# Kernel optimization log

Measured on AMD Instinct MI355X. Metric: run time of the kernel, lower is better.

The kernel has to match this reference:

```python
import jax, jax.numpy as jnp
import numpy as np

LEAK = 0.1   # LeakyReLU negative slope used by Conv2dBatchLeaky
EPS = 1e-5   # BatchNorm eps (torch default)


def conv_bn_leaky(x, w, gamma, beta, mean, var, stride, pad):
    # Conv2d(bias=False) -> BatchNorm (inference) -> LeakyReLU(0.1)
    y = jax.lax.conv_general_dilated(
        x, w, (stride, stride), [(pad, pad), (pad, pad)],
        dimension_numbers=("NCHW", "OIHW", "NCHW"))
    scale = gamma / jnp.sqrt(var + EPS)
    shift = beta - mean * scale
    y = y * scale[None, :, None, None] + shift[None, :, None, None]
    return jnp.where(y > 0, y, LEAK * y)


def reorg(x, s):
    # lightnet Reorg: exact permutation of the darknet reorg layer
    B, C, H, W = x.shape
    x = x.reshape(B, C, H // s, s, W // s, s)
    x = x.transpose(0, 3, 5, 1, 2, 4)           # (B, s, s, C, H/s, W/s)
    return x.reshape(B, s * s * C, H // s, W // s)


def setup_inputs() -> dict:
    key = jax.random.key(0)
    ks = jax.random.split(key, 13)
    B = 64
    inp = {
        "feat0": jax.random.normal(ks[0], (B, 1024, 19, 19), jnp.float32),
        "feat1": jax.random.normal(ks[1], (B, 512, 38, 38), jnp.float32),
        "w1": jax.random.normal(ks[2], (64, 512, 1, 1), jnp.float32) * 0.05,
        "g1": jax.random.uniform(ks[3], (64,), jnp.float32, 0.5, 1.5),
        "b1": jax.random.normal(ks[4], (64,), jnp.float32) * 0.1,
        "m1": jax.random.normal(ks[5], (64,), jnp.float32) * 0.1,
        "v1": jax.random.uniform(ks[6], (64,), jnp.float32, 0.5, 1.5),
        "w2": jax.random.normal(ks[7], (1024, 1280, 3, 3), jnp.float32) * 0.02,
        "g2": jax.random.uniform(ks[8], (1024,), jnp.float32, 0.5, 1.5),
        "b2": jax.random.normal(ks[9], (1024,), jnp.float32) * 0.1,
        "m2": jax.random.normal(ks[10], (1024,), jnp.float32) * 0.1,
        "v2": jax.random.uniform(ks[11], (1024,), jnp.float32, 0.5, 1.5),
        # meta_state: (num_classes=20, num_anchors*6=30, 1024+1)
        "reweight": jax.random.normal(ks[12], (20, 30, 1025), jnp.float32) * 0.05,
    }
    return inp


def reference(feat0, feat1, w1, g1, b1, m1, v1, w2, g2, b2, m2, v2, reweight):
    # layers[0]: 1x1 ConvBatchLeaky(512->64) + Reorg(2)
    x = conv_bn_leaky(feat1, w1, g1, b1, m1, v1, stride=1, pad=0)
    x = reorg(x, 2)                                  # (B, 256, 19, 19)
    # layers[1]: 3x3 ConvBatchLeaky(1280->1024), pad=1
    cat = jnp.concatenate([x, feat0], axis=1)        # (B, 1280, 19, 19)
    pre = conv_bn_leaky(cat, w2, g2, b2, m2, v2, stride=1, pad=1)  # (B,1024,19,19)
    # get_reweighted_output: per-class dynamic 1x1 conv, batched as one einsum
    cw = reweight[:, :, :-1]                         # (K=20, O=30, 1024)
    cb = reweight[:, :, -1]                          # (K, O)
    det = jnp.einsum("bchw,koc->bkohw", pre, cw) + cb[None, :, :, None, None]
    B, _, _, H, W = det.shape
    return det.reshape(B * 20, 30, H, W)
```

## Files before the change

kernel.cpp:

```cpp
#include <hip/hip_runtime.h>

typedef unsigned short u16;
typedef __attribute__((ext_vector_type(8))) __bf16 bf16x8;
typedef __attribute__((ext_vector_type(4))) float f32x4;

__device__ __forceinline__ u16 f2bf(float f) {
  union { float f; unsigned u; } v; v.f = f;
  unsigned r = v.u + 0x7fffu + ((v.u >> 16) & 1u);
  return (u16)(r >> 16);
}

__device__ __forceinline__ void gld16(const void* g, const void* l) {
  __builtin_amdgcn_global_load_lds((const __attribute__((address_space(1))) void*)g,
                                   (__attribute__((address_space(3))) void*)l, 16, 0, 0);
}

#define BARX() do { asm volatile("" ::: "memory"); __builtin_amdgcn_s_barrier(); \
                    asm volatile("" ::: "memory"); } while (0)
#define LGKM0() do { asm volatile("s_waitcnt lgkmcnt(0)" ::: "memory"); \
                     __builtin_amdgcn_sched_barrier(0); } while (0)

__global__ __launch_bounds__(256) void k_prep_small(
    const float* w1, const float* rw,
    const float* g1, const float* b1, const float* m1, const float* v1,
    const float* g2, const float* b2, const float* m2, const float* v2,
    u16* w1b, u16* cwt,
    float* scale1, float* shift1, float* scale2, float* shift2, float* cbf)
{
  int i = blockIdx.x * 256 + threadIdx.x;
  if (i < 32768) { w1b[i] = f2bf(w1[i]); return; }
  i -= 32768;
  if (i < 655360) {
    int n = i >> 10, c = i & 1023;
    cwt[i] = (n < 600) ? f2bf(rw[n * 1025 + c]) : (u16)0;
    return;
  }
  i -= 655360;
  if (i < 64) {
    float s = g1[i] * rsqrtf(v1[i] + 1e-5f);
    scale1[i] = s; shift1[i] = b1[i] - m1[i] * s;
  } else if (i < 1088) {
    int c = i - 64;
    float s = g2[c] * rsqrtf(v2[c] + 1e-5f);
    scale2[c] = s; shift2[c] = b2[c] - m2[c] * s;
  } else if (i < 1728) {
    int n = i - 1088;
    cbf[n] = (n < 600) ? rw[n * 1025 + 1024] : 0.f;
  }
}

__global__ __launch_bounds__(256) void k_prep_w2(const float* w2, u16* w2t) {
  __shared__ float buf[11520];
  int o = blockIdx.x;
  const float* src = w2 + (size_t)o * 11520;
  for (int i = threadIdx.x; i < 11520; i += 256) buf[i] = src[i];
  __syncthreads();
  for (int t = 0; t < 9; ++t) {
    int dy = t / 3, dx = t - dy * 3;
    u16* dst = w2t + ((size_t)dy * 1024 + o) * 3840 + dx * 1280;
    for (int ci = threadIdx.x; ci < 1280; ci += 256) dst[ci] = f2bf(buf[ci * 9 + t]);
  }
}

__global__ __launch_bounds__(256) void k_feat0(const float* feat0, u16* cat) {
  __shared__ float tile[32][33];
  int b = blockIdx.z, c0 = blockIdx.y * 32, p0 = blockIdx.x * 32;
  int tid = threadIdx.x;
  int lo = tid & 31, hi = tid >> 5;
#pragma unroll
  for (int pass = 0; pass < 4; ++pass) {
    int cl = pass * 8 + hi;
    int p = p0 + lo;
    tile[cl][lo] = (p < 361) ? feat0[((size_t)(b * 1024 + c0 + cl)) * 361 + p] : 0.f;
  }
  __syncthreads();
#pragma unroll
  for (int pass = 0; pass < 4; ++pass) {
    int pl = pass * 8 + hi;
    int p = p0 + pl;
    if (p < 361) {
      int h = p / 19, w = p - h * 19;
      cat[(((size_t)b * 21 + 1 + h) * 21 + 1 + w) * 1280 + 256 + c0 + lo] = f2bf(tile[lo][pl]);
    }
  }
}

__global__ __launch_bounds__(256) void k_conv1(const float* feat1, const u16* w1b,
    const float* scale1, const float* shift1, u16* cat)
{
  __shared__ u16 As[128 * 40];
  __shared__ u16 Bs[64 * 32];
  int tid = threadIdx.x;
  int wave = tid >> 6, lane = tid & 63;
  int wr = wave >> 1, wc = wave & 1;
  int lm = lane & 15, lq = lane >> 4;
  int m0 = blockIdx.x * 128;

  int mLoc = tid & 127, cHalf = tid >> 7;
  int mA = m0 + mLoc;
  int bA = mA / 1444, qA = mA - bA * 1444;
  const float* aG = feat1 + ((size_t)bA * 512) * 1444 + qA;

  const u16* bG = w1b + (tid >> 2) * 512 + (tid & 3) * 8;
  char* BsW = (char*)Bs + wave * 1024;

  f32x4 acc[4][2];
#pragma unroll
  for (int i = 0; i < 4; ++i)
#pragma unroll
    for (int j = 0; j < 2; ++j)
#pragma unroll
      for (int r = 0; r < 4; ++r) acc[i][j][r] = 0.f;

  for (int k0 = 0; k0 < 512; k0 += 32) {
    gld16(bG + k0, BsW);
#pragma unroll
    for (int pass = 0; pass < 16; ++pass) {
      int c = pass * 2 + cHalf;
      As[mLoc * 40 + c] = f2bf(aG[(size_t)(k0 + c) * 1444]);
    }
    __syncthreads();
    bf16x8 aF[4], bF[2];
#pragma unroll
    for (int i = 0; i < 4; ++i)
      aF[i] = *(const bf16x8*)(As + (wr * 64 + i * 16 + lm) * 40 + lq * 8);
#pragma unroll
    for (int j = 0; j < 2; ++j)
      bF[j] = *(const bf16x8*)(Bs + (wc * 32 + j * 16 + lm) * 32 + lq * 8);
#pragma unroll
    for (int i = 0; i < 4; ++i)
#pragma unroll
      for (int j = 0; j < 2; ++j)
        acc[i][j] = __builtin_amdgcn_mfma_f32_16x16x32_bf16(aF[i], bF[j], acc[i][j], 0, 0, 0);
    __syncthreads();
  }

  int o0 = wc * 32;
  float sc[2], sh[2];
#pragma unroll
  for (int j = 0; j < 2; ++j) {
    int o = o0 + j * 16 + lm;
    sc[j] = scale1[o]; sh[j] = shift1[o];
  }
#pragma unroll
  for (int i = 0; i < 4; ++i) {
#pragma unroll
    for (int r = 0; r < 4; ++r) {
      int m = m0 + wr * 64 + i * 16 + lq * 4 + r;
      int b = m / 1444, q = m - b * 1444;
      int yy = q / 38, xx = q - yy * 38;
      size_t base = (((size_t)b * 21 + 1 + (yy >> 1)) * 21 + 1 + (xx >> 1)) * 1280
                  + ((yy & 1) * 2 + (xx & 1)) * 64;
#pragma unroll
      for (int j = 0; j < 2; ++j) {
        float v = acc[i][j][r] * sc[j] + sh[j];
        v = v > 0.f ? v : 0.1f * v;
        cat[base + o0 + j * 16 + lm] = f2bf(v);
      }
    }
  }
}

__global__ __launch_bounds__(512) void k_conv2(const u16* cat, const u16* w2t,
    const float* scale2, const float* shift2, u16* pre)
{
  __shared__ __align__(16) u16 As[2][16384];
  __shared__ __align__(16) u16 Bs[2][8192];

  int tid = threadIdx.x;
  int wave = tid >> 6, lane = tid & 63;
  int wr = wave >> 1, wc = wave & 1;
  int lm = lane & 15, lq = lane >> 4;
  int n0 = (blockIdx.x & 7) * 128;
  int m0 = (blockIdx.x >> 3) * 256;

  int rsub = tid >> 3;
  int cOff = ((tid & 7) ^ (rsub & 7)) * 8;

  const u16* aBase[4];
#pragma unroll
  for (int r = 0; r < 4; ++r) {
    int m = m0 + r * 64 + rsub; if (m > 23103) m = 23103;
    int b = m / 361, pq = m - b * 361, y = pq / 19, x = pq - y * 19;
    aBase[r] = cat + ((size_t)(b * 21 + y) * 21 + x) * 1280 + cOff;
  }
  const u16* bBase[2];
#pragma unroll
  for (int r = 0; r < 2; ++r)
    bBase[r] = w2t + (size_t)(n0 + r * 64 + rsub) * 3840 + cOff;

  int c0 = ((0 + lq) ^ (lm & 7)) * 8;
  int c1 = ((4 + lq) ^ (lm & 7)) * 8;
  const u16* aRd = &As[0][(wr * 64 + lm) * 64];
  const u16* bRd = &Bs[0][(wc * 64 + lm) * 64];

  f32x4 acc[4][4];
#pragma unroll
  for (int i = 0; i < 4; ++i)
#pragma unroll
    for (int j = 0; j < 4; ++j)
#pragma unroll
      for (int r = 0; r < 4; ++r) acc[i][j][r] = 0.f;

  auto stageA = [&](int p, int aOff) {
#pragma unroll
    for (int r = 0; r < 4; ++r)
      gld16(aBase[r] + aOff, &As[p][r * 4096 + wave * 512]);
  };
  auto stageB = [&](int p, size_t bOff) {
#pragma unroll
    for (int r = 0; r < 2; ++r)
      gld16(bBase[r] + bOff, &Bs[p][r * 4096 + wave * 512]);
  };

  stageA(0, 0);        stageB(0, 0);
  stageA(1, 64);       stageB(1, 64);
  asm volatile("s_waitcnt vmcnt(6)" ::: "memory");
  __builtin_amdgcn_sched_barrier(0);
  BARX();

  int dyS = 0, koS = 128;

  for (int kt = 0; kt < 180; ++kt) {
    int p = kt & 1;
    const u16* A = aRd + p * 16384;
    const u16* B = bRd + p * 8192;
    bool pf = (kt + 2 < 180);
    int aOff = dyS * 26880 + koS;
    size_t bOff = (size_t)dyS * 3932160 + koS;

    bf16x8 aF[4][2], bF[4][2];

#pragma unroll
    for (int i = 0; i < 2; ++i) {
      aF[i][0] = *(const bf16x8*)(A + i * 1024 + c0);
      aF[i][1] = *(const bf16x8*)(A + i * 1024 + c1);
    }
#pragma unroll
    for (int j = 0; j < 2; ++j) {
      bF[j][0] = *(const bf16x8*)(B + j * 1024 + c0);
      bF[j][1] = *(const bf16x8*)(B + j * 1024 + c1);
    }
    BARX();
    LGKM0();
    __builtin_amdgcn_s_setprio(1);
#pragma unroll
    for (int i = 0; i < 2; ++i)
#pragma unroll
      for (int j = 0; j < 2; ++j) {
        acc[i][j] = __builtin_amdgcn_mfma_f32_16x16x32_bf16(aF[i][0], bF[j][0], acc[i][j], 0, 0, 0);
        acc[i][j] = __builtin_amdgcn_mfma_f32_16x16x32_bf16(aF[i][1], bF[j][1], acc[i][j], 0, 0, 0);
      }
    __builtin_amdgcn_s_setprio(0);
    BARX();

#pragma unroll
    for (int i = 2; i < 4; ++i) {
      aF[i][0] = *(const bf16x8*)(A + i * 1024 + c0);
      aF[i][1] = *(const bf16x8*)(A + i * 1024 + c1);
    }
    BARX();
    LGKM0();
    __builtin_amdgcn_s_setprio(1);
#pragma unroll
    for (int i = 2; i < 4; ++i)
#pragma unroll
      for (int j = 0; j < 2; ++j) {
        acc[i][j] = __builtin_amdgcn_mfma_f32_16x16x32_bf16(aF[i][0], bF[j][0], acc[i][j], 0, 0, 0);
        acc[i][j] = __builtin_amdgcn_mfma_f32_16x16x32_bf16(aF[i][1], bF[j][1], acc[i][j], 0, 0, 0);
      }
    __builtin_amdgcn_s_setprio(0);
    BARX();

#pragma unroll
    for (int j = 2; j < 4; ++j) {
      bF[j][0] = *(const bf16x8*)(B + j * 1024 + c0);
      bF[j][1] = *(const bf16x8*)(B + j * 1024 + c1);
    }
    if (pf) stageA(p, aOff);
    BARX();
    LGKM0();
    __builtin_amdgcn_s_setprio(1);
#pragma unroll
    for (int i = 2; i < 4; ++i)
#pragma unroll
      for (int j = 2; j < 4; ++j) {
        acc[i][j] = __builtin_amdgcn_mfma_f32_16x16x32_bf16(aF[i][0], bF[j][0], acc[i][j], 0, 0, 0);
        acc[i][j] = __builtin_amdgcn_mfma_f32_16x16x32_bf16(aF[i][1], bF[j][1], acc[i][j], 0, 0, 0);
      }
    __builtin_amdgcn_s_setprio(0);
    BARX();

    if (pf) stageB(p, bOff);
    __builtin_amdgcn_s_setprio(1);
#pragma unroll
    for (int i = 0; i < 2; ++i)
#pragma unroll
      for (int j = 2; j < 4; ++j) {
        acc[i][j] = __builtin_amdgcn_mfma_f32_16x16x32_bf16(aF[i][0], bF[j][0], acc[i][j], 0, 0, 0);
        acc[i][j] = __builtin_amdgcn_mfma_f32_16x16x32_bf16(aF[i][1], bF[j][1], acc[i][j], 0, 0, 0);
      }
    __builtin_amdgcn_s_setprio(0);

    koS += 64;
    if (koS == 3840) { koS = 0; ++dyS; }

    if (kt < 179) {
      if (kt == 178) { asm volatile("s_waitcnt vmcnt(0)" ::: "memory"); }
      else           { asm volatile("s_waitcnt vmcnt(6)" ::: "memory"); }
      __builtin_amdgcn_sched_barrier(0);
      BARX();
    }
  }

  int nn[4]; float sc[4], sh[4];
#pragma unroll
  for (int j = 0; j < 4; ++j) {
    nn[j] = n0 + wc * 64 + j * 16 + lm;
    sc[j] = scale2[nn[j]]; sh[j] = shift2[nn[j]];
  }
#pragma unroll
  for (int i = 0; i < 4; ++i) {
#pragma unroll
    for (int r = 0; r < 4; ++r) {
      int m = m0 + wr * 64 + i * 16 + lq * 4 + r;
      if (m < 23104) {
        u16* row = pre + (size_t)m * 1024;
#pragma unroll
        for (int j = 0; j < 4; ++j) {
          float v = acc[i][j][r] * sc[j] + sh[j];
          v = v > 0.f ? v : 0.1f * v;
          row[nn[j]] = f2bf(v);
        }
      }
    }
  }
}

__global__ __launch_bounds__(256) void k_einsum(const u16* pre, const u16* cwt,
    const float* cbf, float* out)
{
  __shared__ u16 As[4096];
  __shared__ u16 Bs[4096];
  int tid = threadIdx.x;
  int wave = tid >> 6, lane = tid & 63;
  int wr = wave >> 1, wc = wave & 1;
  int lm = lane & 15, lq = lane >> 4;
  int m0 = blockIdx.x * 128;
  int n0 = blockIdx.y * 128;

  int r0 = tid >> 2, seg = (tid & 3) * 8;
  const u16* aP0 = cwt + (size_t)(m0 + r0) * 1024 + seg;
  const u16* aP1 = aP0 + (size_t)64 * 1024;
  int q0 = n0 + r0;       if (q0 > 23103) q0 = 23103;
  int q1 = n0 + r0 + 64;  if (q1 > 23103) q1 = 23103;
  const u16* bP0 = pre + (size_t)q0 * 1024 + seg;
  const u16* bP1 = pre + (size_t)q1 * 1024 + seg;

  char* AsW = (char*)As + wave * 1024;
  char* BsW = (char*)Bs + wave * 1024;

  f32x4 acc[4][4];
#pragma unroll
  for (int i = 0; i < 4; ++i)
#pragma unroll
    for (int j = 0; j < 4; ++j)
#pragma unroll
      for (int r = 0; r < 4; ++r) acc[i][j][r] = 0.f;

  for (int k0 = 0; k0 < 1024; k0 += 32) {
    gld16(aP0 + k0, AsW);
    gld16(aP1 + k0, AsW + 4096);
    gld16(bP0 + k0, BsW);
    gld16(bP1 + k0, BsW + 4096);
    __syncthreads();
    bf16x8 aF[4], bF[4];
#pragma unroll
    for (int i = 0; i < 4; ++i)
      aF[i] = *(const bf16x8*)(As + (wr * 64 + i * 16 + lm) * 32 + lq * 8);
#pragma unroll
    for (int j = 0; j < 4; ++j)
      bF[j] = *(const bf16x8*)(Bs + (wc * 64 + j * 16 + lm) * 32 + lq * 8);
#pragma unroll
    for (int i = 0; i < 4; ++i)
#pragma unroll
      for (int j = 0; j < 4; ++j)
        acc[i][j] = __builtin_amdgcn_mfma_f32_16x16x32_bf16(aF[i], bF[j], acc[i][j], 0, 0, 0);
    __syncthreads();
  }

  int pix[4], pb[4], pp[4];
#pragma unroll
  for (int j = 0; j < 4; ++j) {
    pix[j] = n0 + wc * 64 + j * 16 + lm;
    int b = pix[j] / 361;
    pb[j] = b; pp[j] = pix[j] - b * 361;
  }
#pragma unroll
  for (int i = 0; i < 4; ++i) {
#pragma unroll
    for (int r = 0; r < 4; ++r) {
      int cw = m0 + wr * 64 + i * 16 + lq * 4 + r;
      if (cw < 600) {
        float bias = cbf[cw];
#pragma unroll
        for (int j = 0; j < 4; ++j) {
          if (pix[j] < 23104)
            out[(size_t)pb[j] * 216600 + (size_t)cw * 361 + pp[j]] = acc[i][j][r] + bias;
        }
      }
    }
  }
}


extern "C" void kernel_launch(void* const* d_in, const int* in_sizes, int n_in,
                              void* d_out, int out_size, void* d_ws, size_t ws_size,
                              hipStream_t stream) {
  const float* feat0 = (const float*)d_in[0];
  const float* feat1 = (const float*)d_in[1];
  const float* w1 = (const float*)d_in[2];
  const float* g1 = (const float*)d_in[3];
  const float* b1 = (const float*)d_in[4];
  const float* m1 = (const float*)d_in[5];
  const float* v1 = (const float*)d_in[6];
  const float* w2 = (const float*)d_in[7];
  const float* g2 = (const float*)d_in[8];
  const float* b2 = (const float*)d_in[9];
  const float* m2 = (const float*)d_in[10];
  const float* v2 = (const float*)d_in[11];
  const float* rw = (const float*)d_in[12];
  float* out = (float*)d_out;

  char* ws = (char*)d_ws;
  u16* cat    = (u16*)(ws);
  u16* w2t    = (u16*)(ws + 72253440);
  u16* pre    = (u16*)(ws + 95846400);
  u16* w1b    = (u16*)(ws + 143163392);
  u16* cwt    = (u16*)(ws + 143228928);
  float* scale1 = (float*)(ws + 144539648);
  float* shift1 = (float*)(ws + 144539904);
  float* scale2 = (float*)(ws + 144540160);
  float* shift2 = (float*)(ws + 144544256);
  float* cbf    = (float*)(ws + 144548352);

  hipMemsetAsync(cat, 0, 72253440, stream);

  k_prep_small<<<2696, 256, 0, stream>>>(w1, rw, g1, b1, m1, v1, g2, b2, m2, v2,
                                         w1b, cwt, scale1, shift1, scale2, shift2, cbf);
  k_prep_w2<<<1024, 256, 0, stream>>>(w2, w2t);
  k_feat0<<<dim3(12, 32, 64), 256, 0, stream>>>(feat0, cat);
  k_conv1<<<722, 256, 0, stream>>>(feat1, w1b, scale1, shift1, cat);
  k_conv2<<<728, 512, 0, stream>>>(cat, w2t, scale2, shift2, pre);
  k_einsum<<<dim3(5, 181), 256, 0, stream>>>(pre, cwt, cbf, out);
}
```

Before: 1.308 ms.

## Rework conv2 GEMM to 32x32x16 MFMA with 128x128 tiles and split prefetch

The main implicit-GEMM conv kernel changes from 256x128 tiles with 512 threads and 16x16x32 MFMAs to 128x128 tiles with 256 threads, two blocks per CU, and 32x32x16 MFMAs. Each wave's accumulators become 2x2 f32x16 fragments. The B and A stage loads are now issued at different points in the iteration, with one barrier pair per k-step. The aim is to raise MFMA throughput, cut LDS read traffic and barriers, and gain occupancy. The cost is that smaller tiles lower data reuse per block and the grid doubles.

```diff
diff --git a/kernel.cpp b/kernel.cpp
--- a/kernel.cpp
+++ b/kernel.cpp
@@ -3,6 +3,7 @@
 typedef unsigned short u16;
 typedef __attribute__((ext_vector_type(8))) __bf16 bf16x8;
 typedef __attribute__((ext_vector_type(4))) float f32x4;
+typedef __attribute__((ext_vector_type(16))) float f32x16;
 
 __device__ __forceinline__ u16 f2bf(float f) {
   union { float f; unsigned u; } v; v.f = f;
@@ -161,18 +162,18 @@
   }
 }
 
-__global__ __launch_bounds__(512) void k_conv2(const u16* cat, const u16* w2t,
+__global__ __launch_bounds__(256, 2) void k_conv2(const u16* cat, const u16* w2t,
     const float* scale2, const float* shift2, u16* pre)
 {
-  __shared__ __align__(16) u16 As[2][16384];
+  __shared__ __align__(16) u16 As[2][8192];
   __shared__ __align__(16) u16 Bs[2][8192];
 
   int tid = threadIdx.x;
   int wave = tid >> 6, lane = tid & 63;
   int wr = wave >> 1, wc = wave & 1;
-  int lm = lane & 15, lq = lane >> 4;
+  int l31 = lane & 31, lh = lane >> 5, l7 = lane & 7;
   int n0 = (blockIdx.x & 7) * 128;
-  int m0 = (blockIdx.x >> 3) * 256;
+  int m0 = (blockIdx.x >> 3) * 128;
 
   int rsub = tid >> 3;
   int cOff = ((tid & 7) ^ (rsub & 7)) * 8;
@@ -180,157 +181,123 @@
   const u16* aBase[4];
 #pragma unroll
   for (int r = 0; r < 4; ++r) {
-    int m = m0 + r * 64 + rsub; if (m > 23103) m = 23103;
+    int m = m0 + r * 32 + rsub; if (m > 23103) m = 23103;
     int b = m / 361, pq = m - b * 361, y = pq / 19, x = pq - y * 19;
     aBase[r] = cat + ((size_t)(b * 21 + y) * 21 + x) * 1280 + cOff;
   }
-  const u16* bBase[2];
-#pragma unroll
-  for (int r = 0; r < 2; ++r)
-    bBase[r] = w2t + (size_t)(n0 + r * 64 + rsub) * 3840 + cOff;
-
-  int c0 = ((0 + lq) ^ (lm & 7)) * 8;
-  int c1 = ((4 + lq) ^ (lm & 7)) * 8;
-  const u16* aRd = &As[0][(wr * 64 + lm) * 64];
-  const u16* bRd = &Bs[0][(wc * 64 + lm) * 64];
-
-  f32x4 acc[4][4];
-#pragma unroll
-  for (int i = 0; i < 4; ++i)
-#pragma unroll
-    for (int j = 0; j < 4; ++j)
-#pragma unroll
-      for (int r = 0; r < 4; ++r) acc[i][j][r] = 0.f;
-
-  auto stageA = [&](int p, int aOff) {
+  const u16* bBase[4];
+#pragma unroll
+  for (int r = 0; r < 4; ++r)
+    bBase[r] = w2t + (size_t)(n0 + r * 32 + rsub) * 3840 + cOff;
+
+  int cks[4];
+#pragma unroll
+  for (int ks = 0; ks < 4; ++ks) cks[ks] = ((ks * 2 + lh) ^ l7) * 8;
+
+  const int aRow = (wr * 64 + l31) * 64;
+  const int bRow = (wc * 64 + l31) * 64;
+
+  f32x16 acc[2][2];
+#pragma unroll
+  for (int i = 0; i < 2; ++i)
+#pragma unroll
+    for (int j = 0; j < 2; ++j)
+#pragma unroll
+      for (int r = 0; r < 16; ++r) acc[i][j][r] = 0.f;
+
+  auto stageA = [&](int p, int off) {
 #pragma unroll
     for (int r = 0; r < 4; ++r)
-      gld16(aBase[r] + aOff, &As[p][r * 4096 + wave * 512]);
+      gld16(aBase[r] + off, &As[p][r * 2048 + wave * 512]);
   };
-  auto stageB = [&](int p, size_t bOff) {
-#pragma unroll
-    for (int r = 0; r < 2; ++r)
-      gld16(bBase[r] + bOff, &Bs[p][r * 4096 + wave * 512]);
+  auto stageB = [&](int p, size_t off) {
+#pragma unroll
+    for (int r = 0; r < 4; ++r)
+      gld16(bBase[r] + off, &Bs[p][r * 2048 + wave * 512]);
   };
 
-  stageA(0, 0);        stageB(0, 0);
-  stageA(1, 64);       stageB(1, 64);
-  asm volatile("s_waitcnt vmcnt(6)" ::: "memory");
-  __builtin_amdgcn_sched_barrier(0);
-  BARX();
-
-  int dyS = 0, koS = 128;
+  stageA(0, 0);  stageB(0, 0);  stageA(1, 64);
+
+  int dyA = 0, koA = 128;
+  int dyB = 0, koB = 64;
 
   for (int kt = 0; kt < 180; ++kt) {
     int p = kt & 1;
-    const u16* A = aRd + p * 16384;
-    const u16* B = bRd + p * 8192;
-    bool pf = (kt + 2 < 180);
-    int aOff = dyS * 26880 + koS;
-    size_t bOff = (size_t)dyS * 3932160 + koS;
-
-    bf16x8 aF[4][2], bF[4][2];
-
-#pragma unroll
-    for (int i = 0; i < 2; ++i) {
-      aF[i][0] = *(const bf16x8*)(A + i * 1024 + c0);
-      aF[i][1] = *(const bf16x8*)(A + i * 1024 + c1);
-    }
-#pragma unroll
-    for (int j = 0; j < 2; ++j) {
-      bF[j][0] = *(const bf16x8*)(B + j * 1024 + c0);
-      bF[j][1] = *(const bf16x8*)(B + j * 1024 + c1);
-    }
+    if (kt == 179) { asm volatile("s_waitcnt vmcnt(0)" ::: "memory"); }
+    else           { asm volatile("s_waitcnt vmcnt(4)" ::: "memory"); }
+    __builtin_amdgcn_sched_barrier(0);
     BARX();
+
+    if (kt < 179) {
+      stageB(p ^ 1, (size_t)dyB * 3932160 + koB);
+      koB += 64; if (koB == 3840) { koB = 0; ++dyB; }
+    }
+
+    const u16* Ap = &As[p][aRow];
+    const u16* Bp = &Bs[p][bRow];
+    bf16x8 aF[2][4], bF[2][2];
+#pragma unroll
+    for (int i = 0; i < 2; ++i)
+#pragma unroll
+      for (int ks = 0; ks < 4; ++ks)
+        aF[i][ks] = *(const bf16x8*)(Ap + i * 2048 + cks[ks]);
+#pragma unroll
+    for (int j = 0; j < 2; ++j)
+#pragma unroll
+      for (int ks = 0; ks < 2; ++ks)
+        bF[j][ks] = *(const bf16x8*)(Bp + j * 2048 + cks[ks]);
     LGKM0();
     __builtin_amdgcn_s_setprio(1);
 #pragma unroll
-    for (int i = 0; i < 2; ++i)
-#pragma unroll
-      for (int j = 0; j < 2; ++j) {
-        acc[i][j] = __builtin_amdgcn_mfma_f32_16x16x32_bf16(aF[i][0], bF[j][0], acc[i][j], 0, 0, 0);
-        acc[i][j] = __builtin_amdgcn_mfma_f32_16x16x32_bf16(aF[i][1], bF[j][1], acc[i][j], 0, 0, 0);
-      }
+    for (int ks = 0; ks < 2; ++ks)
+#pragma unroll
+      for (int i = 0; i < 2; ++i)
+#pragma unroll
+        for (int j = 0; j < 2; ++j)
+          acc[i][j] = __builtin_amdgcn_mfma_f32_32x32x16_bf16(aF[i][ks], bF[j][ks], acc[i][j], 0, 0, 0);
     __builtin_amdgcn_s_setprio(0);
     BARX();
 
-#pragma unroll
-    for (int i = 2; i < 4; ++i) {
-      aF[i][0] = *(const bf16x8*)(A + i * 1024 + c0);
-      aF[i][1] = *(const bf16x8*)(A + i * 1024 + c1);
-    }
-    BARX();
+    if (kt < 178) {
+      stageA(p, dyA * 26880 + koA);
+      koA += 64; if (koA == 3840) { koA = 0; ++dyA; }
+    }
+#pragma unroll
+    for (int j = 0; j < 2; ++j)
+#pragma unroll
+      for (int ks = 0; ks < 2; ++ks)
+        bF[j][ks] = *(const bf16x8*)(Bp + j * 2048 + cks[2 + ks]);
     LGKM0();
     __builtin_amdgcn_s_setprio(1);
 #pragma unroll
-    for (int i = 2; i < 4; ++i)
-#pragma unroll
-      for (int j = 0; j < 2; ++j) {
-        acc[i][j] = __builtin_amdgcn_mfma_f32_16x16x32_bf16(aF[i][0], bF[j][0], acc[i][j], 0, 0, 0);
-        acc[i][j] = __builtin_amdgcn_mfma_f32_16x16x32_bf16(aF[i][1], bF[j][1], acc[i][j], 0, 0, 0);
-      }
+    for (int ks = 0; ks < 2; ++ks)
+#pragma unroll
+      for (int i = 0; i < 2; ++i)
+#pragma unroll
+        for (int j = 0; j < 2; ++j)
+          acc[i][j] = __builtin_amdgcn_mfma_f32_32x32x16_bf16(aF[i][2 + ks], bF[j][ks], acc[i][j], 0, 0, 0);
     __builtin_amdgcn_s_setprio(0);
-    BARX();
-
-#pragma unroll
-    for (int j = 2; j < 4; ++j) {
-      bF[j][0] = *(const bf16x8*)(B + j * 1024 + c0);
-      bF[j][1] = *(const bf16x8*)(B + j * 1024 + c1);
-    }
-    if (pf) stageA(p, aOff);
-    BARX();
-    LGKM0();
-    __builtin_amdgcn_s_setprio(1);
-#pragma unroll
-    for (int i = 2; i < 4; ++i)
-#pragma unroll
-      for (int j = 2; j < 4; ++j) {
-        acc[i][j] = __builtin_amdgcn_mfma_f32_16x16x32_bf16(aF[i][0], bF[j][0], acc[i][j], 0, 0, 0);
-        acc[i][j] = __builtin_amdgcn_mfma_f32_16x16x32_bf16(aF[i][1], bF[j][1], acc[i][j], 0, 0, 0);
-      }
-    __builtin_amdgcn_s_setprio(0);
-    BARX();
-
-    if (pf) stageB(p, bOff);
-    __builtin_amdgcn_s_setprio(1);
-#pragma unroll
-    for (int i = 0; i < 2; ++i)
-#pragma unroll
-      for (int j = 2; j < 4; ++j) {
-        acc[i][j] = __builtin_amdgcn_mfma_f32_16x16x32_bf16(aF[i][0], bF[j][0], acc[i][j], 0, 0, 0);
-        acc[i][j] = __builtin_amdgcn_mfma_f32_16x16x32_bf16(aF[i][1], bF[j][1], acc[i][j], 0, 0, 0);
-      }
-    __builtin_amdgcn_s_setprio(0);
-
-    koS += 64;
-    if (koS == 3840) { koS = 0; ++dyS; }
-
-    if (kt < 179) {
-      if (kt == 178) { asm volatile("s_waitcnt vmcnt(0)" ::: "memory"); }
-      else           { asm volatile("s_waitcnt vmcnt(6)" ::: "memory"); }
-      __builtin_amdgcn_sched_barrier(0);
-      BARX();
-    }
-  }
-
-  int nn[4]; float sc[4], sh[4];
-#pragma unroll
-  for (int j = 0; j < 4; ++j) {
-    nn[j] = n0 + wc * 64 + j * 16 + lm;
-    sc[j] = scale2[nn[j]]; sh[j] = shift2[nn[j]];
-  }
-#pragma unroll
-  for (int i = 0; i < 4; ++i) {
-#pragma unroll
-    for (int r = 0; r < 4; ++r) {
-      int m = m0 + wr * 64 + i * 16 + lq * 4 + r;
+  }
+
+  float sc[2], sh[2];
+#pragma unroll
+  for (int j = 0; j < 2; ++j) {
+    int n = n0 + wc * 64 + j * 32 + l31;
+    sc[j] = scale2[n]; sh[j] = shift2[n];
+  }
+#pragma unroll
+  for (int i = 0; i < 2; ++i) {
+    int mb = m0 + wr * 64 + i * 32 + 4 * lh;
+#pragma unroll
+    for (int r = 0; r < 16; ++r) {
+      int m = mb + (r & 3) + 8 * (r >> 2);
       if (m < 23104) {
         u16* row = pre + (size_t)m * 1024;
 #pragma unroll
-        for (int j = 0; j < 4; ++j) {
+        for (int j = 0; j < 2; ++j) {
           float v = acc[i][j][r] * sc[j] + sh[j];
           v = v > 0.f ? v : 0.1f * v;
-          row[nn[j]] = f2bf(v);
+          row[n0 + wc * 64 + j * 32 + l31] = f2bf(v);
         }
       }
     }
@@ -451,6 +418,6 @@
   k_prep_w2<<<1024, 256, 0, stream>>>(w2, w2t);
   k_feat0<<<dim3(12, 32, 64), 256, 0, stream>>>(feat0, cat);
   k_conv1<<<722, 256, 0, stream>>>(feat1, w1b, scale1, shift1, cat);
-  k_conv2<<<728, 512, 0, stream>>>(cat, w2t, scale2, shift2, pre);
+  k_conv2<<<1448, 256, 0, stream>>>(cat, w2t, scale2, shift2, pre);
   k_einsum<<<dim3(5, 181), 256, 0, stream>>>(pre, cwt, cbf, out);
 }
```

New measurement: 1.282 ms. About the same (-1.9%).
